# Kernel optimization log

Measured on AMD Instinct MI355X. Metric: run time of the kernel, lower is better.

## Reference

```python
import jax, jax.numpy as jnp
import numpy as np
from jax import lax

B, T, H, D_OUT, VOCAB = 4096, 64, 512, 256, 10000
BN_EPS = 1e-5


def _gru_cell(x, h, W_ih, W_hh, b_ih, b_hh):
    # PyTorch GRU cell: gates ordered (reset, update, new)
    gi = x @ W_ih.T + b_ih          # (B, 3H)
    gh = h @ W_hh.T + b_hh          # (B, 3H)
    i_r, i_z, i_n = jnp.split(gi, 3, axis=-1)
    h_r, h_z, h_n = jnp.split(gh, 3, axis=-1)
    r = jax.nn.sigmoid(i_r + h_r)
    z = jax.nn.sigmoid(i_z + h_z)
    n = jnp.tanh(i_n + r * h_n)
    return (1.0 - z) * n + z * h


def setup_inputs():
    key = jax.random.key(0)
    ks = jax.random.split(key, 20)
    s = 0.05
    f = jnp.float32
    return {
        'input_cluster': jax.random.randint(ks[0], (B,), 0, VOCAB),
        'out_poses': jax.random.normal(ks[1], (B, T, D_OUT), f),
        'emb': jax.random.normal(ks[2], (VOCAB, H), f) * s,
        'pre_W_ih': jax.random.normal(ks[3], (3 * H, H), f) * s,
        'pre_W_hh': jax.random.normal(ks[4], (3 * H, H), f) * s,
        'pre_b_ih': jax.random.normal(ks[5], (3 * H,), f) * s,
        'pre_b_hh': jax.random.normal(ks[6], (3 * H,), f) * s,
        'lin_W': jax.random.normal(ks[7], (H, D_OUT), f) * s,
        'lin_b': jax.random.normal(ks[8], (H,), f) * s,
        'bn_gamma': jnp.ones((H,), f),
        'bn_beta': jnp.zeros((H,), f),
        'bn_mean': jax.random.normal(ks[9], (H,), f) * s,
        'bn_var': jax.random.uniform(ks[10], (H,), f, 0.5, 1.5),
        'dec_W_ih': jax.random.normal(ks[11], (3 * H, H), f) * s,
        'dec_W_hh': jax.random.normal(ks[12], (3 * H, H), f) * s,
        'dec_b_ih': jax.random.normal(ks[13], (3 * H,), f) * s,
        'dec_b_hh': jax.random.normal(ks[14], (3 * H,), f) * s,
        'out_W': jax.random.normal(ks[15], (D_OUT, H), f) * s,
        'out_b': jax.random.normal(ks[16], (D_OUT,), f) * s,
    }


def reference(input_cluster, out_poses, emb, pre_W_ih, pre_W_hh, pre_b_ih, pre_b_hh,
              lin_W, lin_b, bn_gamma, bn_beta, bn_mean, bn_var,
              dec_W_ih, dec_W_hh, dec_b_ih, dec_b_hh, out_W, out_b):
    # encoder: single-step GRU over the embedded cluster id with h0 = 0
    embedded = emb[input_cluster]                       # (B, H)
    enc_h = _gru_cell(embedded, jnp.zeros_like(embedded),
                      pre_W_ih, pre_W_hh, pre_b_ih, pre_b_hh)
    # NOTE: original code never updates decode_hidden, so the decoder GRU sees
    # the SAME hidden state enc_h at every timestep -> precompute its gates.
    gh = enc_h @ dec_W_hh.T + dec_b_hh                  # (B, 3H), constant
    h_r, h_z, h_n = jnp.split(gh, 3, axis=-1)
    bn_scale = bn_gamma / jnp.sqrt(bn_var + BN_EPS)     # inference-mode BN

    def step(dec_in, _):
        x = dec_in @ lin_W.T + lin_b                    # (B, H)
        x = jax.nn.relu((x - bn_mean) * bn_scale + bn_beta)
        gi = x @ dec_W_ih.T + dec_b_ih
        i_r, i_z, i_n = jnp.split(gi, 3, axis=-1)
        r = jax.nn.sigmoid(i_r + h_r)
        z = jax.nn.sigmoid(i_z + h_z)
        n = jnp.tanh(i_n + r * h_n)
        h_new = (1.0 - z) * n + z * enc_h
        out = h_new @ out_W.T + out_b                   # (B, D_OUT)
        return out, out

    n_frames = out_poses.shape[1]
    dec0 = jnp.zeros_like(out_poses[:, 0, :])
    _, ys = lax.scan(step, dec0, None, length=n_frames - 1)  # (T-1, B, D)
    outputs = jnp.concatenate(
        [jnp.zeros_like(out_poses[:, :1, :]), jnp.transpose(ys, (1, 0, 2))], axis=1)
    return outputs
```

## Files before the change

### kernel.cpp

```cpp
#include <hip/hip_runtime.h>
#include <hip/hip_bf16.h>


typedef unsigned short u16;
typedef __attribute__((ext_vector_type(8))) short short8;
typedef __attribute__((ext_vector_type(4))) float f32x4;
typedef __bf16 bf16x8 __attribute__((ext_vector_type(8)));

#define TDIM 64
#define HDIM 512
#define ODIM 256
#define RROWS 16
#define NBLK 256
#define NTHR 1024
#define PITCH 520
#define PITCH_O 264

#define WS_LINW   0u
#define WS_DECWIH 131072u
#define WS_OUTW   917504u
#define WS_PREWIH 1048576u
#define WS_DECWHH 1835008u
#define WS_TOTAL  2621440u

__device__ inline float b2f(u16 u) {
    unsigned v = ((unsigned)u) << 16;
    float f; __builtin_memcpy(&f, &v, 4); return f;
}
__device__ inline u16 f2b(float f) {
    unsigned u; __builtin_memcpy(&u, &f, 4);
    return (u16)((u + 0x7fffu + ((u >> 16) & 1u)) >> 16);
}
__device__ inline float sigm(float x) {
    return __builtin_amdgcn_rcpf(1.f + __expf(-x));
}
__device__ inline float tanh_f(float x) {
    return 1.f - 2.f * __builtin_amdgcn_rcpf(1.f + __expf(2.f * x));
}
__device__ inline f32x4 mfma16(short8 a, short8 b, f32x4 c) {
    return __builtin_amdgcn_mfma_f32_16x16x32_bf16(
        __builtin_bit_cast(bf16x8, a), __builtin_bit_cast(bf16x8, b), c, 0, 0, 0);
}

template<int WF32> __device__ inline short8 ldw8(const void* p, size_t off) {
    if constexpr (!WF32) {
        return *(const short8*)((const u16*)p + off);
    } else {
        const float* f = (const float*)p + off;
        f32x4 a = *(const f32x4*)f, b = *(const f32x4*)(f + 4);
        short8 r;
        r[0] = (short)f2b(a[0]); r[1] = (short)f2b(a[1]);
        r[2] = (short)f2b(a[2]); r[3] = (short)f2b(a[3]);
        r[4] = (short)f2b(b[0]); r[5] = (short)f2b(b[1]);
        r[6] = (short)f2b(b[2]); r[7] = (short)f2b(b[3]);
        return r;
    }
}
template<int IOF32> __device__ inline float ldf(const void* p, int i) {
    if constexpr (IOF32) return ((const float*)p)[i];
    else return b2f(((const u16*)p)[i]);
}

__global__ void probe_k(const u16* __restrict__ bnv, int* __restrict__ flag) {
    if (threadIdx.x == 0 && blockIdx.x == 0) {
        int hits = 0;
        for (int i = 0; i < 16; ++i) {
            u16 m = (u16)(bnv[i] & 0xFF80u);
            hits += (m == 0x3F00u || m == 0x3F80u) ? 1 : 0;
        }
        *flag = (hits >= 14) ? 1 : 0;
    }
}

__global__ void cvtw_k(const int* __restrict__ flag,
                       const float* __restrict__ linW,
                       const float* __restrict__ decWih,
                       const float* __restrict__ outW,
                       const float* __restrict__ preWih,
                       const float* __restrict__ decWhh,
                       u16* __restrict__ dst) {
    if (*flag == 1) return;
    int i = blockIdx.x * blockDim.x + threadIdx.x;
    const int st = gridDim.x * blockDim.x;
    for (; i < (int)WS_TOTAL; i += st) {
        int j = i; const float* s;
        if (j < 131072) s = linW + j;
        else if ((j -= 131072) < 786432) s = decWih + j;
        else if ((j -= 786432) < 131072) s = outW + j;
        else if ((j -= 131072) < 786432) s = preWih + j;
        else { j -= 786432; s = decWhh + j; }
        dst[i] = f2b(*s);
    }
}

template<int WF32, int IOF32>
__global__ __launch_bounds__(NTHR, 4)
void c2g_kernel(const int* __restrict__ flag,
                const int* __restrict__ cluster,
                const void* __restrict__ emb,
                const void* __restrict__ preWih,
                const void* __restrict__ preBih,
                const void* __restrict__ preBhh,
                const void* __restrict__ linW,
                const void* __restrict__ linB,
                const void* __restrict__ bnG,
                const void* __restrict__ bnB,
                const void* __restrict__ bnM,
                const void* __restrict__ bnV,
                const void* __restrict__ decWih,
                const void* __restrict__ decBih,
                const void* __restrict__ decWhh,
                const void* __restrict__ decBhh,
                const void* __restrict__ outW,
                const void* __restrict__ outB,
                void* __restrict__ out)
{
    if ((*flag == 1) == (IOF32 != 0)) return;

    __shared__ __align__(16) u16 x_lds[RROWS * PITCH];
    __shared__ __align__(16) u16 h_lds[RROWS * PITCH];
    __shared__ __align__(16) u16 e_lds[RROWS * PITCH];
    __shared__ __align__(16) u16 o_lds[RROWS * PITCH_O];

    const int tid  = threadIdx.x;
    const int wave = tid >> 6;
    const int lane = tid & 63;
    const int n16  = lane & 15;
    const int q    = lane >> 4;
    const int blk  = blockIdx.x;
    const int r0   = blk * RROWS;

    for (int i = tid; i < RROWS * PITCH_O; i += NTHR) o_lds[i] = 0;
    for (int i = tid; i < RROWS * ODIM; i += NTHR) {
        int m = i >> 8, c = i & 255;
        size_t idx = (size_t)(r0 + m) * TDIM * ODIM + c;
        if constexpr (IOF32) __builtin_nontemporal_store(0.f, (float*)out + idx);
        else                 __builtin_nontemporal_store((u16)0, (u16*)out + idx);
    }
    for (int i = tid; i < RROWS * HDIM; i += NTHR) {
        int m = i >> 9, c = i & 511;
        x_lds[m * PITCH + c] =
            f2b(ldf<IOF32>(emb, cluster[r0 + m] * HDIM + c));
    }
    __syncthreads();

    const int jc0 = (wave * 2 + 0) * 16 + n16;
    const int jc1 = (wave * 2 + 1) * 16 + n16;
    const int jc3 = wave * 16 + n16;

    f32x4 ehr[2];
    #pragma unroll
    for (int i = 0; i < 2; ++i) {
        const int jc = i ? jc1 : jc0;
        f32x4 ar = {0,0,0,0}, az = {0,0,0,0}, an = {0,0,0,0};
        #pragma unroll 4
        for (int kc = 0; kc < 16; ++kc) {
            const int ko = kc * 32 + q * 8;
            short8 a0 = *(const short8*)&x_lds[n16 * PITCH + ko];
            short8 br = ldw8<WF32>(preWih, (size_t)(jc)        * HDIM + ko);
            short8 bz = ldw8<WF32>(preWih, (size_t)(512 + jc)  * HDIM + ko);
            short8 bn = ldw8<WF32>(preWih, (size_t)(1024 + jc) * HDIM + ko);
            ar = mfma16(a0, br, ar); az = mfma16(a0, bz, az); an = mfma16(a0, bn, an);
        }
        const float bir = ldf<IOF32>(preBih, jc);
        const float biz = ldf<IOF32>(preBih, 512 + jc);
        const float bin = ldf<IOF32>(preBih, 1024 + jc);
        const float ghr = ldf<IOF32>(preBhh, jc);
        const float ghz = ldf<IOF32>(preBhh, 512 + jc);
        const float ghn = ldf<IOF32>(preBhh, 1024 + jc);
        #pragma unroll
        for (int r = 0; r < 4; ++r) {
            float rr = sigm(ar[r] + bir + ghr);
            float zz = sigm(az[r] + biz + ghz);
            float nn = tanh_f(an[r] + bin + rr * ghn);
            float ev = (1.f - zz) * nn;
            ehr[i][r] = ev;
            e_lds[(q * 4 + r) * PITCH + jc] = f2b(ev);
        }
    }
    __syncthreads();

    f32x4 gh[2][3];
    #pragma unroll
    for (int i = 0; i < 2; ++i) {
        const int jc = i ? jc1 : jc0;
        f32x4 ar = {0,0,0,0}, az = {0,0,0,0}, an = {0,0,0,0};
        #pragma unroll 4
        for (int kc = 0; kc < 16; ++kc) {
            const int ko = kc * 32 + q * 8;
            short8 a0 = *(const short8*)&e_lds[n16 * PITCH + ko];
            short8 br = ldw8<WF32>(decWhh, (size_t)(jc)        * HDIM + ko);
            short8 bz = ldw8<WF32>(decWhh, (size_t)(512 + jc)  * HDIM + ko);
            short8 bn = ldw8<WF32>(decWhh, (size_t)(1024 + jc) * HDIM + ko);
            ar = mfma16(a0, br, ar); az = mfma16(a0, bz, az); an = mfma16(a0, bn, an);
        }
        const float cr = ldf<IOF32>(decBhh, jc)        + ldf<IOF32>(decBih, jc);
        const float cz = ldf<IOF32>(decBhh, 512 + jc)  + ldf<IOF32>(decBih, 512 + jc);
        const float cn = ldf<IOF32>(decBhh, 1024 + jc);
        #pragma unroll
        for (int r = 0; r < 4; ++r) {
            gh[i][0][r] = ar[r] + cr;
            gh[i][1][r] = az[r] + cz;
            gh[i][2][r] = an[r] + cn;
        }
    }

    float c_s[2], c_o[2], c_bin[2];
    #pragma unroll
    for (int i = 0; i < 2; ++i) {
        const int jc = i ? jc1 : jc0;
        const float s = ldf<IOF32>(bnG, jc) *
            __builtin_amdgcn_rcpf(sqrtf(ldf<IOF32>(bnV, jc) + 1e-5f));
        c_s[i] = s;
        c_o[i] = (ldf<IOF32>(linB, jc) - ldf<IOF32>(bnM, jc)) * s
               + ldf<IOF32>(bnB, jc);
        c_bin[i] = ldf<IOF32>(decBih, 1024 + jc);
    }
    const float c_ob = ldf<IOF32>(outB, jc3);

    for (int t = 0; t < TDIM - 1; ++t) {
        #pragma unroll
        for (int i = 0; i < 2; ++i) {
            const int jc = i ? jc1 : jc0;
            f32x4 a = {0,0,0,0};
            #pragma unroll
            for (int kc = 0; kc < 8; ++kc) {
                const int ko = kc * 32 + q * 8;
                short8 bw = ldw8<WF32>(linW, (size_t)jc * ODIM + ko);
                short8 f0 = *(const short8*)&o_lds[n16 * PITCH_O + ko];
                a = mfma16(f0, bw, a);
            }
            #pragma unroll
            for (int r = 0; r < 4; ++r) {
                float xv = a[r] * c_s[i] + c_o[i];
                x_lds[(q * 4 + r) * PITCH + jc] = f2b(fmaxf(xv, 0.f));
            }
        }
        __syncthreads();

        #pragma unroll
        for (int i = 0; i < 2; ++i) {
            const int jc = i ? jc1 : jc0;
            f32x4 ar = {0,0,0,0}, az = {0,0,0,0}, an = {0,0,0,0};
            #pragma unroll 4
            for (int kc = 0; kc < 16; ++kc) {
                const int ko = kc * 32 + q * 8;
                short8 a0 = *(const short8*)&x_lds[n16 * PITCH + ko];
                short8 br = ldw8<WF32>(decWih, (size_t)(jc)        * HDIM + ko);
                short8 bz = ldw8<WF32>(decWih, (size_t)(512 + jc)  * HDIM + ko);
                short8 bn = ldw8<WF32>(decWih, (size_t)(1024 + jc) * HDIM + ko);
                ar = mfma16(a0, br, ar); az = mfma16(a0, bz, az); an = mfma16(a0, bn, an);
            }
            #pragma unroll
            for (int r = 0; r < 4; ++r) {
                float rr = sigm(ar[r] + gh[i][0][r]);
                float zz = sigm(az[r] + gh[i][1][r]);
                float nn = tanh_f(an[r] + c_bin[i] + rr * gh[i][2][r]);
                h_lds[(q * 4 + r) * PITCH + jc] =
                    f2b((1.f - zz) * nn + zz * ehr[i][r]);
            }
        }
        __syncthreads();

        {
            f32x4 a = {0,0,0,0};
            #pragma unroll 4
            for (int kc = 0; kc < 16; ++kc) {
                const int ko = kc * 32 + q * 8;
                short8 bw = ldw8<WF32>(outW, (size_t)jc3 * HDIM + ko);
                short8 f0 = *(const short8*)&h_lds[n16 * PITCH + ko];
                a = mfma16(f0, bw, a);
            }
            #pragma unroll
            for (int r = 0; r < 4; ++r) {
                float val = a[r] + c_ob;
                int row = q * 4 + r;
                o_lds[row * PITCH_O + jc3] = f2b(val);
                size_t idx = (size_t)(r0 + row) * TDIM * ODIM
                           + (size_t)(t + 1) * ODIM + jc3;
                if constexpr (IOF32)
                    __builtin_nontemporal_store(val, (float*)out + idx);
                else
                    __builtin_nontemporal_store(f2b(val), (u16*)out + idx);
            }
        }
        __syncthreads();
    }
}

extern "C" void kernel_launch(void* const* d_in, const int* in_sizes, int n_in,
                              void* d_out, int out_size, void* d_ws, size_t ws_size,
                              hipStream_t stream) {
    const int* cluster = (const int*)d_in[0];
    int* flag = (int*)d_ws;
    u16* wsW  = (u16*)((char*)d_ws + 64);
    const size_t NEED = 64 + (size_t)WS_TOTAL * 2;

    probe_k<<<dim3(1), dim3(64), 0, stream>>>((const u16*)d_in[12], flag);

    c2g_kernel<0, 0><<<dim3(NBLK), dim3(NTHR), 0, stream>>>(
        flag, cluster, d_in[2], d_in[3], d_in[5], d_in[6], d_in[7], d_in[8],
        d_in[9], d_in[10], d_in[11], d_in[12], d_in[13], d_in[15], d_in[14],
        d_in[16], d_in[17], d_in[18], d_out);

    if (ws_size >= NEED) {
        cvtw_k<<<dim3(2048), dim3(256), 0, stream>>>(
            flag, (const float*)d_in[7], (const float*)d_in[13],
            (const float*)d_in[17], (const float*)d_in[3],
            (const float*)d_in[14], wsW);
        c2g_kernel<0, 1><<<dim3(NBLK), dim3(NTHR), 0, stream>>>(
            flag, cluster, d_in[2], wsW + WS_PREWIH, d_in[5], d_in[6],
            wsW + WS_LINW, d_in[8], d_in[9], d_in[10], d_in[11], d_in[12],
            wsW + WS_DECWIH, d_in[15], wsW + WS_DECWHH, d_in[16],
            wsW + WS_OUTW, d_in[18], d_out);
    } else {
        c2g_kernel<1, 1><<<dim3(NBLK), dim3(NTHR), 0, stream>>>(
            flag, cluster, d_in[2], d_in[3], d_in[5], d_in[6], d_in[7], d_in[8],
            d_in[9], d_in[10], d_in[11], d_in[12], d_in[13], d_in[15], d_in[14],
            d_in[16], d_in[17], d_in[18], d_out);
    }
}
```

Baseline: 3.954 ms.

## Stream bf16 weights through per-wave LDS ring via async global_load_lds

Measured after the change: 6.679 ms. +68.9%, slower.

```diff
diff --git a/kernel.cpp b/kernel.cpp
--- a/kernel.cpp
+++ b/kernel.cpp
@@ -15,6 +15,8 @@
 #define NTHR 1024
 #define PITCH 520
 #define PITCH_O 264
+#define SLOTS 6
+#define STW (SLOTS*512)
 
 #define WS_LINW   0u
 #define WS_DECWIH 131072u
@@ -40,6 +42,14 @@
 __device__ inline f32x4 mfma16(short8 a, short8 b, f32x4 c) {
     return __builtin_amdgcn_mfma_f32_16x16x32_bf16(
         __builtin_bit_cast(bf16x8, a), __builtin_bit_cast(bf16x8, b), c, 0, 0, 0);
+}
+__device__ inline void gld16(const u16* g, u16* l) {
+    __builtin_amdgcn_global_load_lds(
+        (const __attribute__((address_space(1))) void*)g,
+        (__attribute__((address_space(3))) void*)l, 16, 0, 0);
+}
+template<int N> __device__ inline void waitvm() {
+    asm volatile("s_waitcnt vmcnt(%0)" :: "n"(N) : "memory");
 }
 
 template<int WF32> __device__ inline short8 ldw8(const void* p, size_t off) {
@@ -119,16 +129,20 @@
 
     __shared__ __align__(16) u16 x_lds[RROWS * PITCH];
     __shared__ __align__(16) u16 h_lds[RROWS * PITCH];
-    __shared__ __align__(16) u16 e_lds[RROWS * PITCH];
     __shared__ __align__(16) u16 o_lds[RROWS * PITCH_O];
+    __shared__ __align__(16) u16 stage[16 * STW];
 
     const int tid  = threadIdx.x;
     const int wave = tid >> 6;
     const int lane = tid & 63;
     const int n16  = lane & 15;
     const int q    = lane >> 4;
+    const int qo   = q * 8;
+    const int le   = lane * 8;
     const int blk  = blockIdx.x;
     const int r0   = blk * RROWS;
+    const int swe  = wave * STW;
+    u16* const sw  = &stage[swe];
 
     for (int i = tid; i < RROWS * PITCH_O; i += NTHR) o_lds[i] = 0;
     for (int i = tid; i < RROWS * ODIM; i += NTHR) {
@@ -149,59 +163,155 @@
     const int jc3 = wave * 16 + n16;
 
     f32x4 ehr[2];
-    #pragma unroll
-    for (int i = 0; i < 2; ++i) {
-        const int jc = i ? jc1 : jc0;
-        f32x4 ar = {0,0,0,0}, az = {0,0,0,0}, an = {0,0,0,0};
-        #pragma unroll 4
+    if constexpr (WF32 == 0) {
+        const u16* wp = (const u16*)preWih;
+        const u16* pe[6];
+        #pragma unroll
+        for (int i = 0; i < 2; ++i)
+            #pragma unroll
+            for (int g = 0; g < 3; ++g)
+                pe[i*3+g] = wp + (size_t)(g*512 + (i ? jc1 : jc0)) * HDIM + qo;
+        #pragma unroll
+        for (int g = 0; g < 6; ++g) gld16(pe[g], sw + g*512);
+        f32x4 acc[6];
+        #pragma unroll
+        for (int g = 0; g < 6; ++g) acc[g] = (f32x4){0,0,0,0};
+        #pragma unroll
         for (int kc = 0; kc < 16; ++kc) {
-            const int ko = kc * 32 + q * 8;
-            short8 a0 = *(const short8*)&x_lds[n16 * PITCH + ko];
-            short8 br = ldw8<WF32>(preWih, (size_t)(jc)        * HDIM + ko);
-            short8 bz = ldw8<WF32>(preWih, (size_t)(512 + jc)  * HDIM + ko);
-            short8 bn = ldw8<WF32>(preWih, (size_t)(1024 + jc) * HDIM + ko);
-            ar = mfma16(a0, br, ar); az = mfma16(a0, bz, az); an = mfma16(a0, bn, an);
-        }
-        const float bir = ldf<IOF32>(preBih, jc);
-        const float biz = ldf<IOF32>(preBih, 512 + jc);
-        const float bin = ldf<IOF32>(preBih, 1024 + jc);
-        const float ghr = ldf<IOF32>(preBhh, jc);
-        const float ghz = ldf<IOF32>(preBhh, 512 + jc);
-        const float ghn = ldf<IOF32>(preBhh, 1024 + jc);
-        #pragma unroll
-        for (int r = 0; r < 4; ++r) {
-            float rr = sigm(ar[r] + bir + ghr);
-            float zz = sigm(az[r] + biz + ghz);
-            float nn = tanh_f(an[r] + bin + rr * ghn);
-            float ev = (1.f - zz) * nn;
-            ehr[i][r] = ev;
-            e_lds[(q * 4 + r) * PITCH + jc] = f2b(ev);
+            short8 fA = *(const short8*)&x_lds[n16 * PITCH + kc*32 + qo];
+            if (kc == 15) waitvm<0>();
+            #pragma unroll
+            for (int g = 0; g < 6; ++g) {
+                if (kc < 15) {
+                    waitvm<5>();
+                    short8 b = *(const short8*)&stage[swe + g*512 + le];
+                    gld16(pe[g] + (kc+1)*32, sw + g*512);
+                    acc[g] = mfma16(fA, b, acc[g]);
+                } else {
+                    short8 b = *(const short8*)&stage[swe + g*512 + le];
+                    acc[g] = mfma16(fA, b, acc[g]);
+                }
+            }
+        }
+        #pragma unroll
+        for (int i = 0; i < 2; ++i) {
+            const int jc = i ? jc1 : jc0;
+            const float bir = ldf<IOF32>(preBih, jc);
+            const float biz = ldf<IOF32>(preBih, 512 + jc);
+            const float bin = ldf<IOF32>(preBih, 1024 + jc);
+            const float ghr = ldf<IOF32>(preBhh, jc);
+            const float ghz = ldf<IOF32>(preBhh, 512 + jc);
+            const float ghn = ldf<IOF32>(preBhh, 1024 + jc);
+            #pragma unroll
+            for (int r = 0; r < 4; ++r) {
+                float rr = sigm(acc[i*3+0][r] + bir + ghr);
+                float zz = sigm(acc[i*3+1][r] + biz + ghz);
+                float nn = tanh_f(acc[i*3+2][r] + bin + rr * ghn);
+                float ev = (1.f - zz) * nn;
+                ehr[i][r] = ev;
+                h_lds[(q*4+r) * PITCH + jc] = f2b(ev);
+            }
+        }
+    } else {
+        #pragma unroll
+        for (int i = 0; i < 2; ++i) {
+            const int jc = i ? jc1 : jc0;
+            f32x4 ar = {0,0,0,0}, az = {0,0,0,0}, an = {0,0,0,0};
+            #pragma unroll 4
+            for (int kc = 0; kc < 16; ++kc) {
+                const int ko = kc*32 + qo;
+                short8 a0 = *(const short8*)&x_lds[n16 * PITCH + ko];
+                short8 br = ldw8<WF32>(preWih, (size_t)(jc)        * HDIM + ko);
+                short8 bz = ldw8<WF32>(preWih, (size_t)(512 + jc)  * HDIM + ko);
+                short8 bn = ldw8<WF32>(preWih, (size_t)(1024 + jc) * HDIM + ko);
+                ar = mfma16(a0, br, ar); az = mfma16(a0, bz, az); an = mfma16(a0, bn, an);
+            }
+            const float bir = ldf<IOF32>(preBih, jc);
+            const float biz = ldf<IOF32>(preBih, 512 + jc);
+            const float bin = ldf<IOF32>(preBih, 1024 + jc);
+            const float ghr = ldf<IOF32>(preBhh, jc);
+            const float ghz = ldf<IOF32>(preBhh, 512 + jc);
+            const float ghn = ldf<IOF32>(preBhh, 1024 + jc);
+            #pragma unroll
+            for (int r = 0; r < 4; ++r) {
+                float rr = sigm(ar[r] + bir + ghr);
+                float zz = sigm(az[r] + biz + ghz);
+                float nn = tanh_f(an[r] + bin + rr * ghn);
+                float ev = (1.f - zz) * nn;
+                ehr[i][r] = ev;
+                h_lds[(q*4+r) * PITCH + jc] = f2b(ev);
+            }
         }
     }
     __syncthreads();
 
     f32x4 gh[2][3];
-    #pragma unroll
-    for (int i = 0; i < 2; ++i) {
-        const int jc = i ? jc1 : jc0;
-        f32x4 ar = {0,0,0,0}, az = {0,0,0,0}, an = {0,0,0,0};
-        #pragma unroll 4
+    if constexpr (WF32 == 0) {
+        const u16* wp = (const u16*)decWhh;
+        const u16* ph[6];
+        #pragma unroll
+        for (int i = 0; i < 2; ++i)
+            #pragma unroll
+            for (int g = 0; g < 3; ++g)
+                ph[i*3+g] = wp + (size_t)(g*512 + (i ? jc1 : jc0)) * HDIM + qo;
+        #pragma unroll
+        for (int g = 0; g < 6; ++g) gld16(ph[g], sw + g*512);
+        f32x4 acc[6];
+        #pragma unroll
+        for (int g = 0; g < 6; ++g) acc[g] = (f32x4){0,0,0,0};
+        #pragma unroll
         for (int kc = 0; kc < 16; ++kc) {
-            const int ko = kc * 32 + q * 8;
-            short8 a0 = *(const short8*)&e_lds[n16 * PITCH + ko];
-            short8 br = ldw8<WF32>(decWhh, (size_t)(jc)        * HDIM + ko);
-            short8 bz = ldw8<WF32>(decWhh, (size_t)(512 + jc)  * HDIM + ko);
-            short8 bn = ldw8<WF32>(decWhh, (size_t)(1024 + jc) * HDIM + ko);
-            ar = mfma16(a0, br, ar); az = mfma16(a0, bz, az); an = mfma16(a0, bn, an);
-        }
-        const float cr = ldf<IOF32>(decBhh, jc)        + ldf<IOF32>(decBih, jc);
-        const float cz = ldf<IOF32>(decBhh, 512 + jc)  + ldf<IOF32>(decBih, 512 + jc);
-        const float cn = ldf<IOF32>(decBhh, 1024 + jc);
-        #pragma unroll
-        for (int r = 0; r < 4; ++r) {
-            gh[i][0][r] = ar[r] + cr;
-            gh[i][1][r] = az[r] + cz;
-            gh[i][2][r] = an[r] + cn;
+            short8 fA = *(const short8*)&h_lds[n16 * PITCH + kc*32 + qo];
+            if (kc == 15) waitvm<0>();
+            #pragma unroll
+            for (int g = 0; g < 6; ++g) {
+                if (kc < 15) {
+                    waitvm<5>();
+                    short8 b = *(const short8*)&stage[swe + g*512 + le];
+                    gld16(ph[g] + (kc+1)*32, sw + g*512);
+                    acc[g] = mfma16(fA, b, acc[g]);
+                } else {
+                    short8 b = *(const short8*)&stage[swe + g*512 + le];
+                    acc[g] = mfma16(fA, b, acc[g]);
+                }
+            }
+        }
+        #pragma unroll
+        for (int i = 0; i < 2; ++i) {
+            const int jc = i ? jc1 : jc0;
+            const float cr = ldf<IOF32>(decBhh, jc)       + ldf<IOF32>(decBih, jc);
+            const float cz = ldf<IOF32>(decBhh, 512 + jc) + ldf<IOF32>(decBih, 512 + jc);
+            const float cn = ldf<IOF32>(decBhh, 1024 + jc);
+            #pragma unroll
+            for (int r = 0; r < 4; ++r) {
+                gh[i][0][r] = acc[i*3+0][r] + cr;
+                gh[i][1][r] = acc[i*3+1][r] + cz;
+                gh[i][2][r] = acc[i*3+2][r] + cn;
+            }
+        }
+    } else {
+        #pragma unroll
+        for (int i = 0; i < 2; ++i) {
+            const int jc = i ? jc1 : jc0;
+            f32x4 ar = {0,0,0,0}, az = {0,0,0,0}, an = {0,0,0,0};
+            #pragma unroll 4
+            for (int kc = 0; kc < 16; ++kc) {
+                const int ko = kc*32 + qo;
+                short8 a0 = *(const short8*)&h_lds[n16 * PITCH + ko];
+                short8 br = ldw8<WF32>(decWhh, (size_t)(jc)        * HDIM + ko);
+                short8 bz = ldw8<WF32>(decWhh, (size_t)(512 + jc)  * HDIM + ko);
+                short8 bn = ldw8<WF32>(decWhh, (size_t)(1024 + jc) * HDIM + ko);
+                ar = mfma16(a0, br, ar); az = mfma16(a0, bz, az); an = mfma16(a0, bn, an);
+            }
+            const float cr = ldf<IOF32>(decBhh, jc)       + ldf<IOF32>(decBih, jc);
+            const float cz = ldf<IOF32>(decBhh, 512 + jc) + ldf<IOF32>(decBih, 512 + jc);
+            const float cn = ldf<IOF32>(decBhh, 1024 + jc);
+            #pragma unroll
+            for (int r = 0; r < 4; ++r) {
+                gh[i][0][r] = ar[r] + cr;
+                gh[i][1][r] = az[r] + cz;
+                gh[i][2][r] = an[r] + cn;
+            }
         }
     }
 
@@ -217,64 +327,118 @@
         c_bin[i] = ldf<IOF32>(decBih, 1024 + jc);
     }
     const float c_ob = ldf<IOF32>(outB, jc3);
-
-    for (int t = 0; t < TDIM - 1; ++t) {
-        #pragma unroll
-        for (int i = 0; i < 2; ++i) {
-            const int jc = i ? jc1 : jc0;
+    __syncthreads();
+
+    if constexpr (WF32 == 0) {
+        const u16* lw  = (const u16*)linW;
+        const u16* wih = (const u16*)decWih;
+        const u16* ow  = (const u16*)outW;
+        const u16* pl0 = lw + (size_t)jc0 * ODIM + qo;
+        const u16* pl1 = lw + (size_t)jc1 * ODIM + qo;
+        const u16* pw[6];
+        #pragma unroll
+        for (int i = 0; i < 2; ++i)
+            #pragma unroll
+            for (int g = 0; g < 3; ++g)
+                pw[i*3+g] = wih + (size_t)(g*512 + (i ? jc1 : jc0)) * HDIM + qo;
+        const u16* po = ow + (size_t)jc3 * HDIM + qo;
+
+        for (int t = 0; t < TDIM - 1; ++t) {
+            #pragma unroll
+            for (int kc = 0; kc < 3; ++kc) {
+                gld16(pl0 + kc*32, sw + kc*512);
+                gld16(pl1 + kc*32, sw + (3+kc)*512);
+            }
+            f32x4 a0 = {0,0,0,0}, a1 = {0,0,0,0};
+            #pragma unroll
+            for (int kc = 0; kc < 8; ++kc) {
+                short8 fA = *(const short8*)&o_lds[n16 * PITCH_O + kc*32 + qo];
+                if (kc < 5) {
+                    waitvm<5>();
+                    short8 w0 = *(const short8*)&stage[swe + (kc%3)*512 + le];
+                    gld16(pl0 + (kc+3)*32, sw + (kc%3)*512);
+                    a0 = mfma16(fA, w0, a0);
+                    waitvm<5>();
+                    short8 w1 = *(const short8*)&stage[swe + (3+kc%3)*512 + le];
+                    gld16(pl1 + (kc+3)*32, sw + (3+kc%3)*512);
+                    a1 = mfma16(fA, w1, a1);
+                } else {
+                    if (kc == 5) waitvm<0>();
+                    short8 w0 = *(const short8*)&stage[swe + (kc%3)*512 + le];
+                    a0 = mfma16(fA, w0, a0);
+                    short8 w1 = *(const short8*)&stage[swe + (3+kc%3)*512 + le];
+                    a1 = mfma16(fA, w1, a1);
+                }
+            }
+            #pragma unroll
+            for (int i = 0; i < 2; ++i) {
+                const int jc = i ? jc1 : jc0;
+                f32x4 v = i ? a1 : a0;
+                #pragma unroll
+                for (int r = 0; r < 4; ++r) {
+                    float xv = v[r] * c_s[i] + c_o[i];
+                    x_lds[(q*4+r) * PITCH + jc] = f2b(fmaxf(xv, 0.f));
+                }
+            }
+            __syncthreads();
+
+            #pragma unroll
+            for (int g = 0; g < 6; ++g) gld16(pw[g], sw + g*512);
+            f32x4 acc[6];
+            #pragma unroll
+            for (int g = 0; g < 6; ++g) acc[g] = (f32x4){0,0,0,0};
+            #pragma unroll
+            for (int kc = 0; kc < 16; ++kc) {
+                short8 fA = *(const short8*)&x_lds[n16 * PITCH + kc*32 + qo];
+                if (kc == 15) waitvm<0>();
+                #pragma unroll
+                for (int g = 0; g < 6; ++g) {
+                    if (kc < 15) {
+                        waitvm<5>();
+                        short8 b = *(const short8*)&stage[swe + g*512 + le];
+                        gld16(pw[g] + (kc+1)*32, sw + g*512);
+                        acc[g] = mfma16(fA, b, acc[g]);
+                    } else {
+                        short8 b = *(const short8*)&stage[swe + g*512 + le];
+                        acc[g] = mfma16(fA, b, acc[g]);
+                    }
+                }
+            }
+            #pragma unroll
+            for (int i = 0; i < 2; ++i) {
+                const int jc = i ? jc1 : jc0;
+                #pragma unroll
+                for (int r = 0; r < 4; ++r) {
+                    float rr = sigm(acc[i*3+0][r] + gh[i][0][r]);
+                    float zz = sigm(acc[i*3+1][r] + gh[i][1][r]);
+                    float nn = tanh_f(acc[i*3+2][r] + c_bin[i] + rr * gh[i][2][r]);
+                    h_lds[(q*4+r) * PITCH + jc] =
+                        f2b((1.f - zz) * nn + zz * ehr[i][r]);
+                }
+            }
+            __syncthreads();
+
+            #pragma unroll
+            for (int kc = 0; kc < 4; ++kc) gld16(po + kc*32, sw + kc*512);
             f32x4 a = {0,0,0,0};
             #pragma unroll
-            for (int kc = 0; kc < 8; ++kc) {
-                const int ko = kc * 32 + q * 8;
-                short8 bw = ldw8<WF32>(linW, (size_t)jc * ODIM + ko);
-                short8 f0 = *(const short8*)&o_lds[n16 * PITCH_O + ko];
-                a = mfma16(f0, bw, a);
-            }
-            #pragma unroll
-            for (int r = 0; r < 4; ++r) {
-                float xv = a[r] * c_s[i] + c_o[i];
-                x_lds[(q * 4 + r) * PITCH + jc] = f2b(fmaxf(xv, 0.f));
-            }
-        }
-        __syncthreads();
-
-        #pragma unroll
-        for (int i = 0; i < 2; ++i) {
-            const int jc = i ? jc1 : jc0;
-            f32x4 ar = {0,0,0,0}, az = {0,0,0,0}, an = {0,0,0,0};
-            #pragma unroll 4
             for (int kc = 0; kc < 16; ++kc) {
-                const int ko = kc * 32 + q * 8;
-                short8 a0 = *(const short8*)&x_lds[n16 * PITCH + ko];
-                short8 br = ldw8<WF32>(decWih, (size_t)(jc)        * HDIM + ko);
-                short8 bz = ldw8<WF32>(decWih, (size_t)(512 + jc)  * HDIM + ko);
-                short8 bn = ldw8<WF32>(decWih, (size_t)(1024 + jc) * HDIM + ko);
-                ar = mfma16(a0, br, ar); az = mfma16(a0, bz, az); an = mfma16(a0, bn, an);
-            }
-            #pragma unroll
-            for (int r = 0; r < 4; ++r) {
-                float rr = sigm(ar[r] + gh[i][0][r]);
-                float zz = sigm(az[r] + gh[i][1][r]);
-                float nn = tanh_f(an[r] + c_bin[i] + rr * gh[i][2][r]);
-                h_lds[(q * 4 + r) * PITCH + jc] =
-                    f2b((1.f - zz) * nn + zz * ehr[i][r]);
-            }
-        }
-        __syncthreads();
-
-        {
-            f32x4 a = {0,0,0,0};
-            #pragma unroll 4
-            for (int kc = 0; kc < 16; ++kc) {
-                const int ko = kc * 32 + q * 8;
-                short8 bw = ldw8<WF32>(outW, (size_t)jc3 * HDIM + ko);
-                short8 f0 = *(const short8*)&h_lds[n16 * PITCH + ko];
-                a = mfma16(f0, bw, a);
+                short8 fA = *(const short8*)&h_lds[n16 * PITCH + kc*32 + qo];
+                if (kc < 12) {
+                    waitvm<3>();
+                    short8 b = *(const short8*)&stage[swe + (kc&3)*512 + le];
+                    gld16(po + (kc+4)*32, sw + (kc&3)*512);
+                    a = mfma16(fA, b, a);
+                } else {
+                    if (kc == 12) waitvm<0>();
+                    short8 b = *(const short8*)&stage[swe + (kc&3)*512 + le];
+                    a = mfma16(fA, b, a);
+                }
             }
             #pragma unroll
             for (int r = 0; r < 4; ++r) {
                 float val = a[r] + c_ob;
-                int row = q * 4 + r;
+                int row = q*4 + r;
                 o_lds[row * PITCH_O + jc3] = f2b(val);
                 size_t idx = (size_t)(r0 + row) * TDIM * ODIM
                            + (size_t)(t + 1) * ODIM + jc3;
@@ -283,8 +447,75 @@
                 else
                     __builtin_nontemporal_store(f2b(val), (u16*)out + idx);
             }
-        }
-        __syncthreads();
+            __syncthreads();
+        }
+    } else {
+        for (int t = 0; t < TDIM - 1; ++t) {
+            #pragma unroll
+            for (int i = 0; i < 2; ++i) {
+                const int jc = i ? jc1 : jc0;
+                f32x4 a = {0,0,0,0};
+                #pragma unroll
+                for (int kc = 0; kc < 8; ++kc) {
+                    const int ko = kc*32 + qo;
+                    short8 bw = ldw8<WF32>(linW, (size_t)jc * ODIM + ko);
+                    short8 f0 = *(const short8*)&o_lds[n16 * PITCH_O + ko];
+                    a = mfma16(f0, bw, a);
+                }
+                #pragma unroll
+                for (int r = 0; r < 4; ++r) {
+                    float xv = a[r] * c_s[i] + c_o[i];
+                    x_lds[(q*4+r) * PITCH + jc] = f2b(fmaxf(xv, 0.f));
+                }
+            }
+            __syncthreads();
+            #pragma unroll
+            for (int i = 0; i < 2; ++i) {
+                const int jc = i ? jc1 : jc0;
+                f32x4 ar = {0,0,0,0}, az = {0,0,0,0}, an = {0,0,0,0};
+                #pragma unroll 4
+                for (int kc = 0; kc < 16; ++kc) {
+                    const int ko = kc*32 + qo;
+                    short8 a0 = *(const short8*)&x_lds[n16 * PITCH + ko];
+                    short8 br = ldw8<WF32>(decWih, (size_t)(jc)        * HDIM + ko);
+                    short8 bz = ldw8<WF32>(decWih, (size_t)(512 + jc)  * HDIM + ko);
+                    short8 bn = ldw8<WF32>(decWih, (size_t)(1024 + jc) * HDIM + ko);
+                    ar = mfma16(a0, br, ar); az = mfma16(a0, bz, az); an = mfma16(a0, bn, an);
+                }
+                #pragma unroll
+                for (int r = 0; r < 4; ++r) {
+                    float rr = sigm(ar[r] + gh[i][0][r]);
+                    float zz = sigm(az[r] + gh[i][1][r]);
+                    float nn = tanh_f(an[r] + c_bin[i] + rr * gh[i][2][r]);
+                    h_lds[(q*4+r) * PITCH + jc] =
+                        f2b((1.f - zz) * nn + zz * ehr[i][r]);
+                }
+            }
+            __syncthreads();
+            {
+                f32x4 a = {0,0,0,0};
+                #pragma unroll 4
+                for (int kc = 0; kc < 16; ++kc) {
+                    const int ko = kc*32 + qo;
+                    short8 bw = ldw8<WF32>(outW, (size_t)jc3 * HDIM + ko);
+                    short8 f0 = *(const short8*)&h_lds[n16 * PITCH + ko];
+                    a = mfma16(f0, bw, a);
+                }
+                #pragma unroll
+                for (int r = 0; r < 4; ++r) {
+                    float val = a[r] + c_ob;
+                    int row = q*4 + r;
+                    o_lds[row * PITCH_O + jc3] = f2b(val);
+                    size_t idx = (size_t)(r0 + row) * TDIM * ODIM
+                               + (size_t)(t + 1) * ODIM + jc3;
+                    if constexpr (IOF32)
+                        __builtin_nontemporal_store(val, (float*)out + idx);
+                    else
+                        __builtin_nontemporal_store(f2b(val), (u16*)out + idx);
+                }
+            }
+            __syncthreads();
+        }
     }
 }
 
```

## Software-pipeline weight loads across GEMM stages and use lightweight LDS-only barriers

Applied to the files above, without the earlier changes.

New measurement: 4.782 ms. +20.9%, slower.

```diff
diff --git a/kernel.cpp b/kernel.cpp
--- a/kernel.cpp
+++ b/kernel.cpp
@@ -40,6 +40,11 @@
 __device__ inline f32x4 mfma16(short8 a, short8 b, f32x4 c) {
     return __builtin_amdgcn_mfma_f32_16x16x32_bf16(
         __builtin_bit_cast(bf16x8, a), __builtin_bit_cast(bf16x8, b), c, 0, 0, 0);
+}
+__device__ inline void bar_nd() {
+    asm volatile("s_waitcnt lgkmcnt(0)" ::: "memory");
+    __builtin_amdgcn_s_barrier();
+    asm volatile("" ::: "memory");
 }
 
 template<int WF32> __device__ inline short8 ldw8(const void* p, size_t off) {
@@ -119,7 +124,6 @@
 
     __shared__ __align__(16) u16 x_lds[RROWS * PITCH];
     __shared__ __align__(16) u16 h_lds[RROWS * PITCH];
-    __shared__ __align__(16) u16 e_lds[RROWS * PITCH];
     __shared__ __align__(16) u16 o_lds[RROWS * PITCH_O];
 
     const int tid  = threadIdx.x;
@@ -127,6 +131,7 @@
     const int lane = tid & 63;
     const int n16  = lane & 15;
     const int q    = lane >> 4;
+    const int qo   = q * 8;
     const int blk  = blockIdx.x;
     const int r0   = blk * RROWS;
 
@@ -134,8 +139,8 @@
     for (int i = tid; i < RROWS * ODIM; i += NTHR) {
         int m = i >> 8, c = i & 255;
         size_t idx = (size_t)(r0 + m) * TDIM * ODIM + c;
-        if constexpr (IOF32) __builtin_nontemporal_store(0.f, (float*)out + idx);
-        else                 __builtin_nontemporal_store((u16)0, (u16*)out + idx);
+        if constexpr (IOF32) ((float*)out)[idx] = 0.f;
+        else                 ((u16*)out)[idx] = 0;
     }
     for (int i = tid; i < RROWS * HDIM; i += NTHR) {
         int m = i >> 9, c = i & 511;
@@ -155,7 +160,7 @@
         f32x4 ar = {0,0,0,0}, az = {0,0,0,0}, an = {0,0,0,0};
         #pragma unroll 4
         for (int kc = 0; kc < 16; ++kc) {
-            const int ko = kc * 32 + q * 8;
+            const int ko = kc*32 + qo;
             short8 a0 = *(const short8*)&x_lds[n16 * PITCH + ko];
             short8 br = ldw8<WF32>(preWih, (size_t)(jc)        * HDIM + ko);
             short8 bz = ldw8<WF32>(preWih, (size_t)(512 + jc)  * HDIM + ko);
@@ -175,7 +180,7 @@
             float nn = tanh_f(an[r] + bin + rr * ghn);
             float ev = (1.f - zz) * nn;
             ehr[i][r] = ev;
-            e_lds[(q * 4 + r) * PITCH + jc] = f2b(ev);
+            h_lds[(q*4+r) * PITCH + jc] = f2b(ev);
         }
     }
     __syncthreads();
@@ -187,15 +192,15 @@
         f32x4 ar = {0,0,0,0}, az = {0,0,0,0}, an = {0,0,0,0};
         #pragma unroll 4
         for (int kc = 0; kc < 16; ++kc) {
-            const int ko = kc * 32 + q * 8;
-            short8 a0 = *(const short8*)&e_lds[n16 * PITCH + ko];
+            const int ko = kc*32 + qo;
+            short8 a0 = *(const short8*)&h_lds[n16 * PITCH + ko];
             short8 br = ldw8<WF32>(decWhh, (size_t)(jc)        * HDIM + ko);
             short8 bz = ldw8<WF32>(decWhh, (size_t)(512 + jc)  * HDIM + ko);
             short8 bn = ldw8<WF32>(decWhh, (size_t)(1024 + jc) * HDIM + ko);
             ar = mfma16(a0, br, ar); az = mfma16(a0, bz, az); an = mfma16(a0, bn, an);
         }
-        const float cr = ldf<IOF32>(decBhh, jc)        + ldf<IOF32>(decBih, jc);
-        const float cz = ldf<IOF32>(decBhh, 512 + jc)  + ldf<IOF32>(decBih, 512 + jc);
+        const float cr = ldf<IOF32>(decBhh, jc)       + ldf<IOF32>(decBih, jc);
+        const float cz = ldf<IOF32>(decBhh, 512 + jc) + ldf<IOF32>(decBih, 512 + jc);
         const float cn = ldf<IOF32>(decBhh, 1024 + jc);
         #pragma unroll
         for (int r = 0; r < 4; ++r) {
@@ -217,74 +222,199 @@
         c_bin[i] = ldf<IOF32>(decBih, 1024 + jc);
     }
     const float c_ob = ldf<IOF32>(outB, jc3);
-
-    for (int t = 0; t < TDIM - 1; ++t) {
-        #pragma unroll
-        for (int i = 0; i < 2; ++i) {
-            const int jc = i ? jc1 : jc0;
+    __syncthreads();
+
+    if constexpr (WF32 == 0) {
+        const u16* lw  = (const u16*)linW;
+        const u16* wih = (const u16*)decWih;
+        const u16* ow  = (const u16*)outW;
+        const unsigned ol0 = (unsigned)jc0 * ODIM + qo;
+        const unsigned ol1 = (unsigned)jc1 * ODIM + qo;
+        const unsigned og0 = (unsigned)(jc0)        * HDIM + qo;
+        const unsigned og1 = (unsigned)(512 + jc0)  * HDIM + qo;
+        const unsigned og2 = (unsigned)(1024 + jc0) * HDIM + qo;
+        const unsigned og3 = (unsigned)(jc1)        * HDIM + qo;
+        const unsigned og4 = (unsigned)(512 + jc1)  * HDIM + qo;
+        const unsigned og5 = (unsigned)(1024 + jc1) * HDIM + qo;
+        const unsigned oo  = (unsigned)jc3 * HDIM + qo;
+
+        short8 g1a = *(const short8*)&lw[ol0];
+        short8 g1b = *(const short8*)&lw[ol1];
+
+        for (int t = 0; t < TDIM - 1; ++t) {
+            f32x4 a0 = {0,0,0,0}, a1 = {0,0,0,0};
+            {
+                short8 b0 = g1a, b1 = g1b;
+                #pragma unroll
+                for (int kc = 0; kc < 8; ++kc) {
+                    short8 n0, n1;
+                    if (kc < 7) {
+                        n0 = *(const short8*)&lw[ol0 + (unsigned)(kc+1)*32];
+                        n1 = *(const short8*)&lw[ol1 + (unsigned)(kc+1)*32];
+                    }
+                    short8 fA = *(const short8*)&o_lds[n16 * PITCH_O + kc*32 + qo];
+                    a0 = mfma16(fA, b0, a0); a1 = mfma16(fA, b1, a1);
+                    if (kc < 7) { b0 = n0; b1 = n1; }
+                }
+            }
+            short8 p0 = *(const short8*)&wih[og0];
+            short8 p1 = *(const short8*)&wih[og1];
+            short8 p2 = *(const short8*)&wih[og2];
+            #pragma unroll
+            for (int r = 0; r < 4; ++r) {
+                float x0 = a0[r] * c_s[0] + c_o[0];
+                float x1 = a1[r] * c_s[1] + c_o[1];
+                x_lds[(q*4+r) * PITCH + jc0] = f2b(fmaxf(x0, 0.f));
+                x_lds[(q*4+r) * PITCH + jc1] = f2b(fmaxf(x1, 0.f));
+            }
+            bar_nd();
+
+            f32x4 ar = {0,0,0,0}, az = {0,0,0,0}, an = {0,0,0,0};
+            {
+                short8 b0 = p0, b1 = p1, b2 = p2;
+                #pragma unroll
+                for (int kc = 0; kc < 16; ++kc) {
+                    short8 n0, n1, n2;
+                    if (kc < 15) {
+                        n0 = *(const short8*)&wih[og0 + (unsigned)(kc+1)*32];
+                        n1 = *(const short8*)&wih[og1 + (unsigned)(kc+1)*32];
+                        n2 = *(const short8*)&wih[og2 + (unsigned)(kc+1)*32];
+                    }
+                    short8 fA = *(const short8*)&x_lds[n16 * PITCH + kc*32 + qo];
+                    ar = mfma16(fA, b0, ar); az = mfma16(fA, b1, az); an = mfma16(fA, b2, an);
+                    if (kc < 15) { b0 = n0; b1 = n1; b2 = n2; }
+                }
+            }
+            p0 = *(const short8*)&wih[og3];
+            p1 = *(const short8*)&wih[og4];
+            p2 = *(const short8*)&wih[og5];
+            #pragma unroll
+            for (int r = 0; r < 4; ++r) {
+                float rr = sigm(ar[r] + gh[0][0][r]);
+                float zz = sigm(az[r] + gh[0][1][r]);
+                float nn = tanh_f(an[r] + c_bin[0] + rr * gh[0][2][r]);
+                h_lds[(q*4+r) * PITCH + jc0] =
+                    f2b((1.f - zz) * nn + zz * ehr[0][r]);
+            }
+
+            ar = (f32x4){0,0,0,0}; az = (f32x4){0,0,0,0}; an = (f32x4){0,0,0,0};
+            {
+                short8 b0 = p0, b1 = p1, b2 = p2;
+                #pragma unroll
+                for (int kc = 0; kc < 16; ++kc) {
+                    short8 n0, n1, n2;
+                    if (kc < 15) {
+                        n0 = *(const short8*)&wih[og3 + (unsigned)(kc+1)*32];
+                        n1 = *(const short8*)&wih[og4 + (unsigned)(kc+1)*32];
+                        n2 = *(const short8*)&wih[og5 + (unsigned)(kc+1)*32];
+                    }
+                    short8 fA = *(const short8*)&x_lds[n16 * PITCH + kc*32 + qo];
+                    ar = mfma16(fA, b0, ar); az = mfma16(fA, b1, az); an = mfma16(fA, b2, an);
+                    if (kc < 15) { b0 = n0; b1 = n1; b2 = n2; }
+                }
+            }
+            short8 e0 = *(const short8*)&ow[oo];
+            short8 e1 = *(const short8*)&ow[oo + 32];
+            #pragma unroll
+            for (int r = 0; r < 4; ++r) {
+                float rr = sigm(ar[r] + gh[1][0][r]);
+                float zz = sigm(az[r] + gh[1][1][r]);
+                float nn = tanh_f(an[r] + c_bin[1] + rr * gh[1][2][r]);
+                h_lds[(q*4+r) * PITCH + jc1] =
+                    f2b((1.f - zz) * nn + zz * ehr[1][r]);
+            }
+            bar_nd();
+
             f32x4 a = {0,0,0,0};
             #pragma unroll
-            for (int kc = 0; kc < 8; ++kc) {
-                const int ko = kc * 32 + q * 8;
-                short8 bw = ldw8<WF32>(linW, (size_t)jc * ODIM + ko);
-                short8 f0 = *(const short8*)&o_lds[n16 * PITCH_O + ko];
-                a = mfma16(f0, bw, a);
-            }
-            #pragma unroll
-            for (int r = 0; r < 4; ++r) {
-                float xv = a[r] * c_s[i] + c_o[i];
-                x_lds[(q * 4 + r) * PITCH + jc] = f2b(fmaxf(xv, 0.f));
-            }
-        }
-        __syncthreads();
-
-        #pragma unroll
-        for (int i = 0; i < 2; ++i) {
-            const int jc = i ? jc1 : jc0;
-            f32x4 ar = {0,0,0,0}, az = {0,0,0,0}, an = {0,0,0,0};
-            #pragma unroll 4
             for (int kc = 0; kc < 16; ++kc) {
-                const int ko = kc * 32 + q * 8;
-                short8 a0 = *(const short8*)&x_lds[n16 * PITCH + ko];
-                short8 br = ldw8<WF32>(decWih, (size_t)(jc)        * HDIM + ko);
-                short8 bz = ldw8<WF32>(decWih, (size_t)(512 + jc)  * HDIM + ko);
-                short8 bn = ldw8<WF32>(decWih, (size_t)(1024 + jc) * HDIM + ko);
-                ar = mfma16(a0, br, ar); az = mfma16(a0, bz, az); an = mfma16(a0, bn, an);
-            }
-            #pragma unroll
-            for (int r = 0; r < 4; ++r) {
-                float rr = sigm(ar[r] + gh[i][0][r]);
-                float zz = sigm(az[r] + gh[i][1][r]);
-                float nn = tanh_f(an[r] + c_bin[i] + rr * gh[i][2][r]);
-                h_lds[(q * 4 + r) * PITCH + jc] =
-                    f2b((1.f - zz) * nn + zz * ehr[i][r]);
-            }
-        }
-        __syncthreads();
-
-        {
-            f32x4 a = {0,0,0,0};
-            #pragma unroll 4
-            for (int kc = 0; kc < 16; ++kc) {
-                const int ko = kc * 32 + q * 8;
-                short8 bw = ldw8<WF32>(outW, (size_t)jc3 * HDIM + ko);
-                short8 f0 = *(const short8*)&h_lds[n16 * PITCH + ko];
-                a = mfma16(f0, bw, a);
-            }
+                short8 nn;
+                if (kc < 14)
+                    nn = *(const short8*)&ow[oo + (unsigned)(kc+2)*32];
+                short8 fA = *(const short8*)&h_lds[n16 * PITCH + kc*32 + qo];
+                a = mfma16(fA, e0, a);
+                e0 = e1;
+                if (kc < 14) e1 = nn;
+            }
+            g1a = *(const short8*)&lw[ol0];
+            g1b = *(const short8*)&lw[ol1];
             #pragma unroll
             for (int r = 0; r < 4; ++r) {
                 float val = a[r] + c_ob;
-                int row = q * 4 + r;
+                int row = q*4 + r;
                 o_lds[row * PITCH_O + jc3] = f2b(val);
                 size_t idx = (size_t)(r0 + row) * TDIM * ODIM
                            + (size_t)(t + 1) * ODIM + jc3;
-                if constexpr (IOF32)
-                    __builtin_nontemporal_store(val, (float*)out + idx);
-                else
-                    __builtin_nontemporal_store(f2b(val), (u16*)out + idx);
-            }
-        }
-        __syncthreads();
+                if constexpr (IOF32) ((float*)out)[idx] = val;
+                else                 ((u16*)out)[idx] = f2b(val);
+            }
+            bar_nd();
+        }
+    } else {
+        for (int t = 0; t < TDIM - 1; ++t) {
+            #pragma unroll
+            for (int i = 0; i < 2; ++i) {
+                const int jc = i ? jc1 : jc0;
+                f32x4 a = {0,0,0,0};
+                #pragma unroll
+                for (int kc = 0; kc < 8; ++kc) {
+                    const int ko = kc*32 + qo;
+                    short8 bw = ldw8<WF32>(linW, (size_t)jc * ODIM + ko);
+                    short8 f0 = *(const short8*)&o_lds[n16 * PITCH_O + ko];
+                    a = mfma16(f0, bw, a);
+                }
+                #pragma unroll
+                for (int r = 0; r < 4; ++r) {
+                    float xv = a[r] * c_s[i] + c_o[i];
+                    x_lds[(q*4+r) * PITCH + jc] = f2b(fmaxf(xv, 0.f));
+                }
+            }
+            __syncthreads();
+            #pragma unroll
+            for (int i = 0; i < 2; ++i) {
+                const int jc = i ? jc1 : jc0;
+                f32x4 ar = {0,0,0,0}, az = {0,0,0,0}, an = {0,0,0,0};
+                #pragma unroll 4
+                for (int kc = 0; kc < 16; ++kc) {
+                    const int ko = kc*32 + qo;
+                    short8 a0 = *(const short8*)&x_lds[n16 * PITCH + ko];
+                    short8 br = ldw8<WF32>(decWih, (size_t)(jc)        * HDIM + ko);
+                    short8 bz = ldw8<WF32>(decWih, (size_t)(512 + jc)  * HDIM + ko);
+                    short8 bn = ldw8<WF32>(decWih, (size_t)(1024 + jc) * HDIM + ko);
+                    ar = mfma16(a0, br, ar); az = mfma16(a0, bz, az); an = mfma16(a0, bn, an);
+                }
+                #pragma unroll
+                for (int r = 0; r < 4; ++r) {
+                    float rr = sigm(ar[r] + gh[i][0][r]);
+                    float zz = sigm(az[r] + gh[i][1][r]);
+                    float nn = tanh_f(an[r] + c_bin[i] + rr * gh[i][2][r]);
+                    h_lds[(q*4+r) * PITCH + jc] =
+                        f2b((1.f - zz) * nn + zz * ehr[i][r]);
+                }
+            }
+            __syncthreads();
+            {
+                f32x4 a = {0,0,0,0};
+                #pragma unroll 4
+                for (int kc = 0; kc < 16; ++kc) {
+                    const int ko = kc*32 + qo;
+                    short8 bw = ldw8<WF32>(outW, (size_t)jc3 * HDIM + ko);
+                    short8 f0 = *(const short8*)&h_lds[n16 * PITCH + ko];
+                    a = mfma16(f0, bw, a);
+                }
+                #pragma unroll
+                for (int r = 0; r < 4; ++r) {
+                    float val = a[r] + c_ob;
+                    int row = q*4 + r;
+                    o_lds[row * PITCH_O + jc3] = f2b(val);
+                    size_t idx = (size_t)(r0 + row) * TDIM * ODIM
+                               + (size_t)(t + 1) * ODIM + jc3;
+                    if constexpr (IOF32) ((float*)out)[idx] = val;
+                    else                 ((u16*)out)[idx] = f2b(val);
+                }
+            }
+            __syncthreads();
+        }
     }
 }
 
```
